# Kernel tuning notes

Hardware: AMD Instinct MI355X
Metric: run time of the kernel (lower is better)

## Reference

```python
import jax, jax.numpy as jnp
import numpy as np

# ---- constants mirroring init_kwargs ----
S = 128          # sheet_units
KA = 25          # aff_cf_units
C = 2            # aff_cf_channels
KL = 25          # lat_cf_units
EXC = 9          # exc_units
DA = 1           # aff_cf_dilation
DL = 1           # lat_cf_dilation
HOMEO_TARGET = 0.04
STRENGTH = 1.0

# ---- radial helper masks (get_circle / get_radial_cos) ----
def _dist(n):
    g = jnp.arange(n, dtype=jnp.float32) - (n - 1) / 2.0
    return jnp.sqrt(g[:, None] ** 2 + g[None, :] ** 2)

def _circle(n, r):
    return (_dist(n) < r).astype(jnp.float32)

def _rcos(n, wl):
    return jnp.cos(_dist(n) * jnp.pi / wl)

# afferent envelope: [C*KA*KA], channel-major like torch repeat+view
_ae = _rcos(KA, KA) ** 2 * _circle(KA, KA / 2)
_ae = _ae / _ae.max()
AFF_ENV = jnp.tile(_ae.reshape(1, KA * KA), (C, 1)).reshape(C * KA * KA)

# lateral (LRI) envelope: [KL*KL]
_inh = _rcos(KL, EXC / DL) ** 2 * _circle(KL, EXC / (2 * DL))
_le = _rcos(KL, KL) ** 2 * (1.0 - _inh) * _circle(KL, KL / 2)
LRI_ENV = (_le / _le.max()).reshape(KL * KL)

def _unfold(x, k, dil):
    """x: [C,H,W] -> patches [L, C*k*k], torch F.unfold ordering (C slowest)."""
    Cc, H, W = x.shape
    out = H - dil * (k - 1)
    idx = jnp.arange(out)[:, None] + dil * jnp.arange(k)[None, :]  # [out,k]
    p = x[:, idx, :]          # [C,out,k,W]
    p = p[:, :, :, idx]       # [C,out,k,out,k]
    p = p.transpose(1, 3, 0, 2, 4)  # [out_i,out_j,C,ki,kj]
    return p.reshape(out * out, Cc * k * k)

def setup_inputs() -> dict:
    key = jax.random.key(0)
    k1, k2 = jax.random.split(key)
    in_size = S + DA * (KA - 1)  # 152
    x = jax.random.uniform(k1, (1, C, in_size, in_size), dtype=jnp.float32)
    rfs = jax.random.uniform(k2, (S * S, C * KA * KA, 1), dtype=jnp.float32)
    rfs = rfs / rfs.sum(1, keepdims=True)
    lat_weights = jnp.ones((S * S, KL * KL, 1), jnp.float32) / (KL * KL)
    adathresh = jnp.zeros((1, 1, S, S), jnp.float32)
    return {"x": x, "rfs": rfs, "lat_weights": lat_weights, "adathresh": adathresh}

def _forward(x, rfs, lat_weights, adathresh):
    relu = jax.nn.relu
    rfs = relu(rfs)                 # no_grad positive clamp of params
    lw = relu(lat_weights)
    # afferent: unfold + envelope + per-pixel dot (bmm with [L,F,1])
    tiles = _unfold(x[0], KA, DA) * AFF_ENV[None, :]          # [L, C*KA*KA]
    raw_aff = jnp.einsum('lf,lf->l', tiles, rfs[:, :, 0]).reshape(S, S)
    aff = jax.lax.stop_gradient(raw_aff) - adathresh[0, 0]
    lat = relu(aff)
    # lateral inhibition: pad so unfold yields S*S positions
    p = DL * (KL - 1) // 2
    lt = _unfold(jnp.pad(lat, p)[None], KL, DL) * LRI_ENV[None, :]  # [L, KL*KL]
    lat_neg = jnp.einsum('lf,lf->l', lt, jax.lax.stop_gradient(lw)[:, :, 0]).reshape(S, S)
    lat = lat - lat_neg
    lat = jnp.tanh(relu(lat * STRENGTH + aff))
    # hebbian lateral correlations term (learning_flag path)
    lt2 = _unfold(jnp.pad(lat, p, constant_values=HOMEO_TARGET)[None], KL, DL) * LRI_ENV[None, :]
    weighted = lt2 * lat.reshape(S * S, 1)
    lat_correlations = jnp.einsum('lf,lf->', weighted, lw[:, :, 0])
    return (raw_aff.reshape(1, 1, S, S), lat.reshape(1, 1, S, S),
            lat_correlations, tiles[:, None, :])

def reference(x, rfs, lat_weights, adathresh):
    return _forward(x, rfs, lat_weights, adathresh)
```

## Files before the change

kernel.cpp:

```cpp
#include <hip/hip_runtime.h>
#include <math.h>

#define S 128
#define KA 25
#define KL 25
#define PATCH (KA * KA)
#define FEAT (2 * PATCH)
#define PI_F 3.14159265358979323846f

#define WS_ENV 0
#define WS_LAT0 640
#define WS_PART 17024

__global__ __launch_bounds__(256) void k_tiles_aff(const float* __restrict__ x,
                                                   const float* __restrict__ rfs,
                                                   const float* __restrict__ ada,
                                                   float* __restrict__ raw_aff,
                                                   float* __restrict__ tiles,
                                                   float* __restrict__ ws) {
    __shared__ float s_ae[PATCH];
    __shared__ float s_part[4];
    const int tid = threadIdx.x;
    const int lane = tid & 63;
    const int wv = tid >> 6;

    for (int i = tid; i < PATCH; i += 256) {
        float di = (float)(i / KA) - 12.0f;
        float dj = (float)(i % KA) - 12.0f;
        float d = sqrtf(di * di + dj * dj);
        float v = 0.0f;
        if (d < 12.5f) {
            float c = cosf(d * (PI_F / 25.0f));
            v = c * c;
        }
        s_ae[i] = v;
    }
    __syncthreads();

    const int l = blockIdx.x;
    const int li = l >> 7;
    const int lj = l & 127;
    const long base = (long)l * FEAT;

    float acc = 0.0f;
    for (int f = tid; f < FEAT; f += 256) {
        int c = (f >= PATCH) ? 1 : 0;
        int r = f - c * PATCH;
        int ki = r / KA;
        int kj = r - ki * KA;
        float xv = x[c * (152 * 152) + (li + ki) * 152 + (lj + kj)];
        float t = xv * s_ae[r];
        tiles[base + f] = t;
        acc += t * fmaxf(rfs[base + f], 0.0f);
    }

    for (int off = 32; off > 0; off >>= 1) acc += __shfl_down(acc, off);
    if (lane == 0) s_part[wv] = acc;
    __syncthreads();
    if (tid == 0) {
        float ra = s_part[0] + s_part[1] + s_part[2] + s_part[3];
        raw_aff[l] = ra;
        ws[WS_LAT0 + l] = fmaxf(ra - ada[l], 0.0f);
    }

    if (blockIdx.x == 0) {
        __syncthreads();
        float m = 0.0f;
        for (int i = tid; i < PATCH; i += 256) {
            float di = (float)(i / KL) - 12.0f;
            float dj = (float)(i % KL) - 12.0f;
            float d = sqrtf(di * di + dj * dj);
            float v = 0.0f;
            if (d < 12.5f) {
                float c1 = cosf(d * (PI_F / 25.0f));
                float inh = 0.0f;
                if (d < 4.5f) {
                    float c2 = cosf(d * (PI_F / 9.0f));
                    inh = c2 * c2;
                }
                v = c1 * c1 * (1.0f - inh);
            }
            s_ae[i] = v;
            m = fmaxf(m, v);
        }
        for (int off = 32; off > 0; off >>= 1) m = fmaxf(m, __shfl_down(m, off));
        if (lane == 0) s_part[wv] = m;
        __syncthreads();
        float inv = 1.0f / fmaxf(fmaxf(s_part[0], s_part[1]),
                                 fmaxf(s_part[2], s_part[3]));
        for (int i = tid; i < PATCH; i += 256) ws[WS_ENV + i] = s_ae[i] * inv;
    }
}

__global__ __launch_bounds__(256) void k_lat(const float* __restrict__ raw_aff,
                                             const float* __restrict__ ada,
                                             const float* __restrict__ lw,
                                             float* __restrict__ latf,
                                             const float* __restrict__ ws) {
    __shared__ float s_le[PATCH];
    const int tid = threadIdx.x;
    for (int i = tid; i < PATCH; i += 256) s_le[i] = ws[WS_ENV + i];
    __syncthreads();

    const int lane = tid & 63;
    const int wv = tid >> 6;
    const int l = blockIdx.x * 4 + wv;
    const int li = l >> 7;
    const int lj = l & 127;
    const long base = (long)l * PATCH;
    const float* __restrict__ lat0 = ws + WS_LAT0;

    float acc = 0.0f;
    for (int f = lane; f < PATCH; f += 64) {
        int ki = f / KL;
        int kj = f - ki * KL;
        int ri = li + ki - 12;
        int rj = lj + kj - 12;
        float lv = 0.0f;
        if (ri >= 0 && ri < S && rj >= 0 && rj < S) lv = lat0[ri * S + rj];
        acc += lv * s_le[f] * fmaxf(lw[base + f], 0.0f);
    }
    for (int off = 32; off > 0; off >>= 1) acc += __shfl_down(acc, off);

    if (lane == 0) {
        float aff_l = raw_aff[l] - ada[l];
        float lat0_l = fmaxf(aff_l, 0.0f);
        float v = (lat0_l - acc)  + aff_l;
        latf[l] = tanhf(fmaxf(v, 0.0f));
    }
}

__global__ __launch_bounds__(256) void k_corr(const float* __restrict__ latf,
                                              const float* __restrict__ lw,
                                              float* __restrict__ ws) {
    __shared__ float s_le[PATCH];
    __shared__ float s_part[4];
    const int tid = threadIdx.x;
    for (int i = tid; i < PATCH; i += 256) s_le[i] = ws[WS_ENV + i];
    __syncthreads();

    const int lane = tid & 63;
    const int wv = tid >> 6;
    const int l = blockIdx.x * 4 + wv;
    const int li = l >> 7;
    const int lj = l & 127;
    const long base = (long)l * PATCH;

    float acc = 0.0f;
    for (int f = lane; f < PATCH; f += 64) {
        int ki = f / KL;
        int kj = f - ki * KL;
        int ri = li + ki - 12;
        int rj = lj + kj - 12;
        float lv = 0.04f;
        if (ri >= 0 && ri < S && rj >= 0 && rj < S) lv = latf[ri * S + rj];
        acc += lv * s_le[f] * fmaxf(lw[base + f], 0.0f);
    }
    for (int off = 32; off > 0; off >>= 1) acc += __shfl_down(acc, off);

    if (lane == 0) s_part[wv] = acc * latf[l];
    __syncthreads();
    if (tid == 0)
        ws[WS_PART + blockIdx.x] = s_part[0] + s_part[1] + s_part[2] + s_part[3];
}

__global__ __launch_bounds__(256) void k_reduce(const float* __restrict__ ws,
                                                float* __restrict__ corr) {
    __shared__ float s_part[4];
    const int tid = threadIdx.x;
    const int lane = tid & 63;
    const int wv = tid >> 6;
    float acc = 0.0f;
    for (int i = tid; i < 4096; i += 256) acc += ws[WS_PART + i];
    for (int off = 32; off > 0; off >>= 1) acc += __shfl_down(acc, off);
    if (lane == 0) s_part[wv] = acc;
    __syncthreads();
    if (tid == 0) corr[0] = s_part[0] + s_part[1] + s_part[2] + s_part[3];
}

extern "C" void kernel_launch(void* const* d_in, const int* in_sizes, int n_in,
                              void* d_out, int out_size, void* d_ws, size_t ws_size,
                              hipStream_t stream) {
    const float* x   = (const float*)d_in[0];
    const float* rfs = (const float*)d_in[1];
    const float* lw  = (const float*)d_in[2];
    const float* ada = (const float*)d_in[3];

    float* out      = (float*)d_out;
    float* raw_aff  = out;
    float* latf     = out + S * S;
    float* corr     = out + 2 * S * S;
    float* tiles    = out + 2 * S * S + 1;
    float* ws       = (float*)d_ws;

    k_tiles_aff<<<S * S, 256, 0, stream>>>(x, rfs, ada, raw_aff, tiles, ws);
    k_lat<<<(S * S) / 4, 256, 0, stream>>>(raw_aff, ada, lw, latf, ws);
    k_corr<<<(S * S) / 4, 256, 0, stream>>>(latf, lw, ws);
    k_reduce<<<1, 256, 0, stream>>>(ws, corr);
}
```

Measured before the change: 229.7 us.

## Fuse all stages into one cooperative persistent kernel with vectorized loads

Replaces four kernel launches with a single cooperative kernel that uses grid-wide syncs between the afferent, lateral and correlation stages. Pixels are processed in pairs per wave so rfs and lateral weights can be read as float4, and zero- or target-padded lateral maps in workspace remove bounds checks. The tiles output is written separately with aligned float4 stores. The aim is lower launch overhead and better memory bandwidth use, at the cost of grid syncs, the reads of x done twice, and a dependence on all 1024 blocks being co-resident.

```diff
diff --git a/kernel.cpp b/kernel.cpp
--- a/kernel.cpp
+++ b/kernel.cpp
@@ -1,181 +1,271 @@
 #include <hip/hip_runtime.h>
+#include <hip/hip_cooperative_groups.h>
 #include <math.h>
+
+namespace cg = cooperative_groups;
 
 #define S 128
 #define KA 25
-#define KL 25
-#define PATCH (KA * KA)
-#define FEAT (2 * PATCH)
+#define PATCH 625
+#define FEAT 1250
 #define PI_F 3.14159265358979323846f
-
-#define WS_ENV 0
-#define WS_LAT0 640
-#define WS_PART 17024
-
-__global__ __launch_bounds__(256) void k_tiles_aff(const float* __restrict__ x,
-                                                   const float* __restrict__ rfs,
-                                                   const float* __restrict__ ada,
-                                                   float* __restrict__ raw_aff,
-                                                   float* __restrict__ tiles,
-                                                   float* __restrict__ ws) {
-    __shared__ float s_ae[PATCH];
-    __shared__ float s_part[4];
+#define PADW 152
+#define PADA (PADW * PADW)
+
+#define NBLK 1024
+#define NTHR 256
+#define NWAVE 4096
+#define NPAIR 8192
+
+#define WS_LAT0P 0
+#define WS_LATFP 23168
+#define WS_PART 46336
+
+#define NTILE 20480000
+#define NF4T 5119999
+
+__device__ __forceinline__ int div25(int r) { return (r * 10486) >> 18; }
+__device__ __forceinline__ int woff(int r) { return r + 127 * div25(r); }
+__device__ __forceinline__ int eslot(int r) { return (r & 3) * 160 + (r >> 2); }
+
+__global__ __launch_bounds__(NTHR, 4) void k_all(const float* __restrict__ x,
+                                                 const float* __restrict__ rfs,
+                                                 const float* __restrict__ lw,
+                                                 const float* __restrict__ ada,
+                                                 float* __restrict__ raw_aff,
+                                                 float* __restrict__ latf,
+                                                 float* __restrict__ corr,
+                                                 float* __restrict__ tiles,
+                                                 float* __restrict__ ws) {
+    cg::grid_group grid = cg::this_grid();
+    __shared__ float s_ae[640];
+    __shared__ float s_le[640];
+    __shared__ float s_red[4];
+
     const int tid = threadIdx.x;
     const int lane = tid & 63;
     const int wv = tid >> 6;
-
-    for (int i = tid; i < PATCH; i += 256) {
-        float di = (float)(i / KA) - 12.0f;
-        float dj = (float)(i % KA) - 12.0f;
+    const int bid = blockIdx.x;
+    const int gid = bid * NTHR + tid;
+    const int wid = bid * 4 + wv;
+
+    float m = 0.0f;
+    for (int r = tid; r < PATCH; r += NTHR) {
+        int qi = div25(r);
+        float di = (float)qi - 12.0f;
+        float dj = (float)(r - 25 * qi) - 12.0f;
         float d = sqrtf(di * di + dj * dj);
-        float v = 0.0f;
+        float ae = 0.0f, le = 0.0f;
         if (d < 12.5f) {
-            float c = cosf(d * (PI_F / 25.0f));
-            v = c * c;
-        }
-        s_ae[i] = v;
-    }
+            float c1 = cosf(d * (PI_F / 25.0f));
+            ae = c1 * c1;
+            float inh = 0.0f;
+            if (d < 4.5f) {
+                float c2 = cosf(d * (PI_F / 9.0f));
+                inh = c2 * c2;
+            }
+            le = c1 * c1 * (1.0f - inh);
+        }
+        s_ae[eslot(r)] = ae;
+        s_le[eslot(r)] = le;
+        m = fmaxf(m, le);
+    }
+    if (tid < 12) {
+        int q = tid / 3, t = 157 + tid - 3 * q;
+        s_ae[q * 160 + t] = 0.0f;
+        s_le[q * 160 + t] = 0.0f;
+    }
+    for (int o = 32; o; o >>= 1) m = fmaxf(m, __shfl_down(m, o));
+    if (!lane) s_red[wv] = m;
     __syncthreads();
-
-    const int l = blockIdx.x;
-    const int li = l >> 7;
-    const int lj = l & 127;
-    const long base = (long)l * FEAT;
-
-    float acc = 0.0f;
-    for (int f = tid; f < FEAT; f += 256) {
+    {
+        float inv = 1.0f / fmaxf(fmaxf(s_red[0], s_red[1]),
+                                 fmaxf(s_red[2], s_red[3]));
+        for (int s = tid; s < 640; s += NTHR) s_le[s] *= inv;
+    }
+    for (int i = gid; i < PADA; i += NBLK * NTHR) {
+        int pi = i / PADW, pj = i - pi * PADW;
+        if (pi < 12 || pi >= 140 || pj < 12 || pj >= 140) {
+            ws[WS_LAT0P + i] = 0.0f;
+            ws[WS_LATFP + i] = 0.04f;
+        }
+    }
+    __syncthreads();
+
+    for (int p = wid; p < NPAIR; p += NWAVE) {
+        const int l0 = 2 * p;
+        const int li = l0 >> 7, lj = l0 & 127;
+        const int wb = li * PADW + lj;
+        const long B = (long)l0 * FEAT;
+        float aA = 0.0f, aB = 0.0f;
+        for (int k = lane; k < 625; k += 64) {
+            const float4 rv = *reinterpret_cast<const float4*>(rfs + B + 4 * (long)k);
+#pragma unroll
+            for (int j = 0; j < 4; ++j) {
+                int f = 4 * k + j;
+                int row1 = (f >= FEAT) ? 1 : 0;
+                int g = f - row1 * FEAT;
+                int c = (g >= PATCH) ? 1 : 0;
+                int r = g - c * PATCH;
+                float t = x[c * PADA + wb + row1 + woff(r)] * s_ae[eslot(r)];
+                float v = t * fmaxf((&rv.x)[j], 0.0f);
+                aA += row1 ? 0.0f : v;
+                aB += row1 ? v : 0.0f;
+            }
+        }
+        for (int o = 32; o; o >>= 1) {
+            aA += __shfl_down(aA, o);
+            aB += __shfl_down(aB, o);
+        }
+        if (!lane) {
+            raw_aff[l0]     = aA;
+            raw_aff[l0 + 1] = aB;
+            int pc = (li + 12) * PADW + (lj + 12);
+            ws[WS_LAT0P + pc]     = fmaxf(aA - ada[l0],     0.0f);
+            ws[WS_LAT0P + pc + 1] = fmaxf(aB - ada[l0 + 1], 0.0f);
+        }
+    }
+
+    for (long k = gid; k < NF4T; k += (long)NBLK * NTHR) {
+        long i0 = 3 + (k << 2);
+        float4 v;
+#pragma unroll
+        for (int j = 0; j < 4; ++j) {
+            unsigned int e = (unsigned int)(i0 + j);
+            unsigned int l = e / 1250u;
+            int f = (int)(e - l * 1250u);
+            int c = (f >= PATCH) ? 1 : 0;
+            int r = f - c * PATCH;
+            int li2 = (int)(l >> 7), lj2 = (int)(l & 127u);
+            (&v.x)[j] = x[c * PADA + li2 * PADW + lj2 + woff(r)] * s_ae[eslot(r)];
+        }
+        *reinterpret_cast<float4*>(tiles + i0) = v;
+    }
+    if (gid < 4) {
+        unsigned int e = (gid < 3) ? (unsigned int)gid : (NTILE - 1u);
+        unsigned int l = e / 1250u;
+        int f = (int)(e - l * 1250u);
         int c = (f >= PATCH) ? 1 : 0;
         int r = f - c * PATCH;
-        int ki = r / KA;
-        int kj = r - ki * KA;
-        float xv = x[c * (152 * 152) + (li + ki) * 152 + (lj + kj)];
-        float t = xv * s_ae[r];
-        tiles[base + f] = t;
-        acc += t * fmaxf(rfs[base + f], 0.0f);
-    }
-
-    for (int off = 32; off > 0; off >>= 1) acc += __shfl_down(acc, off);
-    if (lane == 0) s_part[wv] = acc;
+        int li2 = (int)(l >> 7), lj2 = (int)(l & 127u);
+        tiles[e] = x[c * PADA + li2 * PADW + lj2 + woff(r)] * s_ae[eslot(r)];
+    }
+
+    grid.sync();
+
+    auto lat_pair = [&](int p) -> float2 {
+        const int l0 = 2 * p;
+        const int li = l0 >> 7, lj = l0 & 127;
+        const int wb = li * PADW + lj;
+        const long B = (long)p * FEAT;
+        const int peel = (p & 1) ? 2 : 0;
+        const float* __restrict__ plat0 = ws + WS_LAT0P;
+        float aA = 0.0f, aB = 0.0f;
+        if (lane < peel) {
+            int f = lane;
+            aA += plat0[wb + f] * s_le[eslot(f)] * fmaxf(lw[B + f], 0.0f);
+        }
+        for (int k = lane; k < 312; k += 64) {
+            int f0 = peel + 4 * k;
+            const float4 w4 = *reinterpret_cast<const float4*>(lw + B + f0);
+#pragma unroll
+            for (int j = 0; j < 4; ++j) {
+                int f = f0 + j;
+                int row1 = (f >= PATCH) ? 1 : 0;
+                int r = f - row1 * PATCH;
+                float gv = plat0[wb + row1 + woff(r)];
+                float v = gv * s_le[eslot(r)] * fmaxf((&w4.x)[j], 0.0f);
+                aA += row1 ? 0.0f : v;
+                aB += row1 ? v : 0.0f;
+            }
+        }
+        if (peel == 0 && lane < 2) {
+            int f = 1248 + lane;
+            int r = f - PATCH;
+            aB += plat0[wb + 1 + woff(r)] * s_le[eslot(r)] * fmaxf(lw[B + f], 0.0f);
+        }
+        for (int o = 32; o; o >>= 1) {
+            aA += __shfl_down(aA, o);
+            aB += __shfl_down(aB, o);
+        }
+        float2 lv = {0.0f, 0.0f};
+        if (!lane) {
+            float af0 = raw_aff[l0] - ada[l0];
+            float L0 = tanhf(fmaxf(fmaxf(af0, 0.0f) - aA + af0, 0.0f));
+            float af1 = raw_aff[l0 + 1] - ada[l0 + 1];
+            float L1 = tanhf(fmaxf(fmaxf(af1, 0.0f) - aB + af1, 0.0f));
+            latf[l0]     = L0;
+            latf[l0 + 1] = L1;
+            int pc = (li + 12) * PADW + (lj + 12);
+            ws[WS_LATFP + pc]     = L0;
+            ws[WS_LATFP + pc + 1] = L1;
+            lv.x = L0; lv.y = L1;
+        }
+        return lv;
+    };
+    const float2 lvA = lat_pair(wid);
+    const float2 lvB = lat_pair(wid + NWAVE);
+
+    grid.sync();
+
+    auto corr_pair = [&](int p) -> float2 {
+        const int l0 = 2 * p;
+        const int li = l0 >> 7, lj = l0 & 127;
+        const int wb = li * PADW + lj;
+        const long B = (long)p * FEAT;
+        const int peel = (p & 1) ? 2 : 0;
+        const float* __restrict__ platf = ws + WS_LATFP;
+        float aA = 0.0f, aB = 0.0f;
+        if (lane < peel) {
+            int f = lane;
+            aA += platf[wb + f] * s_le[eslot(f)] * fmaxf(lw[B + f], 0.0f);
+        }
+        for (int k = lane; k < 312; k += 64) {
+            int f0 = peel + 4 * k;
+            const float4 w4 = *reinterpret_cast<const float4*>(lw + B + f0);
+#pragma unroll
+            for (int j = 0; j < 4; ++j) {
+                int f = f0 + j;
+                int row1 = (f >= PATCH) ? 1 : 0;
+                int r = f - row1 * PATCH;
+                float gv = platf[wb + row1 + woff(r)];
+                float v = gv * s_le[eslot(r)] * fmaxf((&w4.x)[j], 0.0f);
+                aA += row1 ? 0.0f : v;
+                aB += row1 ? v : 0.0f;
+            }
+        }
+        if (peel == 0 && lane < 2) {
+            int f = 1248 + lane;
+            int r = f - PATCH;
+            aB += platf[wb + 1 + woff(r)] * s_le[eslot(r)] * fmaxf(lw[B + f], 0.0f);
+        }
+        for (int o = 32; o; o >>= 1) {
+            aA += __shfl_down(aA, o);
+            aB += __shfl_down(aB, o);
+        }
+        return {aA, aB};
+    };
+    const float2 cA = corr_pair(wid);
+    const float2 cB = corr_pair(wid + NWAVE);
+
+    float wsum = 0.0f;
+    if (!lane)
+        wsum = cA.x * lvA.x + cA.y * lvA.y + cB.x * lvB.x + cB.y * lvB.y;
+    if (!lane) s_red[wv] = wsum;
     __syncthreads();
-    if (tid == 0) {
-        float ra = s_part[0] + s_part[1] + s_part[2] + s_part[3];
-        raw_aff[l] = ra;
-        ws[WS_LAT0 + l] = fmaxf(ra - ada[l], 0.0f);
-    }
-
-    if (blockIdx.x == 0) {
+    if (!tid)
+        ws[WS_PART + bid] = s_red[0] + s_red[1] + s_red[2] + s_red[3];
+
+    grid.sync();
+
+    if (bid == 0) {
+        float a = 0.0f;
+        for (int i = tid; i < NBLK; i += NTHR) a += ws[WS_PART + i];
+        for (int o = 32; o; o >>= 1) a += __shfl_down(a, o);
+        if (!lane) s_red[wv] = a;
         __syncthreads();
-        float m = 0.0f;
-        for (int i = tid; i < PATCH; i += 256) {
-            float di = (float)(i / KL) - 12.0f;
-            float dj = (float)(i % KL) - 12.0f;
-            float d = sqrtf(di * di + dj * dj);
-            float v = 0.0f;
-            if (d < 12.5f) {
-                float c1 = cosf(d * (PI_F / 25.0f));
-                float inh = 0.0f;
-                if (d < 4.5f) {
-                    float c2 = cosf(d * (PI_F / 9.0f));
-                    inh = c2 * c2;
-                }
-                v = c1 * c1 * (1.0f - inh);
-            }
-            s_ae[i] = v;
-            m = fmaxf(m, v);
-        }
-        for (int off = 32; off > 0; off >>= 1) m = fmaxf(m, __shfl_down(m, off));
-        if (lane == 0) s_part[wv] = m;
-        __syncthreads();
-        float inv = 1.0f / fmaxf(fmaxf(s_part[0], s_part[1]),
-                                 fmaxf(s_part[2], s_part[3]));
-        for (int i = tid; i < PATCH; i += 256) ws[WS_ENV + i] = s_ae[i] * inv;
-    }
-}
-
-__global__ __launch_bounds__(256) void k_lat(const float* __restrict__ raw_aff,
-                                             const float* __restrict__ ada,
-                                             const float* __restrict__ lw,
-                                             float* __restrict__ latf,
-                                             const float* __restrict__ ws) {
-    __shared__ float s_le[PATCH];
-    const int tid = threadIdx.x;
-    for (int i = tid; i < PATCH; i += 256) s_le[i] = ws[WS_ENV + i];
-    __syncthreads();
-
-    const int lane = tid & 63;
-    const int wv = tid >> 6;
-    const int l = blockIdx.x * 4 + wv;
-    const int li = l >> 7;
-    const int lj = l & 127;
-    const long base = (long)l * PATCH;
-    const float* __restrict__ lat0 = ws + WS_LAT0;
-
-    float acc = 0.0f;
-    for (int f = lane; f < PATCH; f += 64) {
-        int ki = f / KL;
-        int kj = f - ki * KL;
-        int ri = li + ki - 12;
-        int rj = lj + kj - 12;
-        float lv = 0.0f;
-        if (ri >= 0 && ri < S && rj >= 0 && rj < S) lv = lat0[ri * S + rj];
-        acc += lv * s_le[f] * fmaxf(lw[base + f], 0.0f);
-    }
-    for (int off = 32; off > 0; off >>= 1) acc += __shfl_down(acc, off);
-
-    if (lane == 0) {
-        float aff_l = raw_aff[l] - ada[l];
-        float lat0_l = fmaxf(aff_l, 0.0f);
-        float v = (lat0_l - acc)  + aff_l;
-        latf[l] = tanhf(fmaxf(v, 0.0f));
-    }
-}
-
-__global__ __launch_bounds__(256) void k_corr(const float* __restrict__ latf,
-                                              const float* __restrict__ lw,
-                                              float* __restrict__ ws) {
-    __shared__ float s_le[PATCH];
-    __shared__ float s_part[4];
-    const int tid = threadIdx.x;
-    for (int i = tid; i < PATCH; i += 256) s_le[i] = ws[WS_ENV + i];
-    __syncthreads();
-
-    const int lane = tid & 63;
-    const int wv = tid >> 6;
-    const int l = blockIdx.x * 4 + wv;
-    const int li = l >> 7;
-    const int lj = l & 127;
-    const long base = (long)l * PATCH;
-
-    float acc = 0.0f;
-    for (int f = lane; f < PATCH; f += 64) {
-        int ki = f / KL;
-        int kj = f - ki * KL;
-        int ri = li + ki - 12;
-        int rj = lj + kj - 12;
-        float lv = 0.04f;
-        if (ri >= 0 && ri < S && rj >= 0 && rj < S) lv = latf[ri * S + rj];
-        acc += lv * s_le[f] * fmaxf(lw[base + f], 0.0f);
-    }
-    for (int off = 32; off > 0; off >>= 1) acc += __shfl_down(acc, off);
-
-    if (lane == 0) s_part[wv] = acc * latf[l];
-    __syncthreads();
-    if (tid == 0)
-        ws[WS_PART + blockIdx.x] = s_part[0] + s_part[1] + s_part[2] + s_part[3];
-}
-
-__global__ __launch_bounds__(256) void k_reduce(const float* __restrict__ ws,
-                                                float* __restrict__ corr) {
-    __shared__ float s_part[4];
-    const int tid = threadIdx.x;
-    const int lane = tid & 63;
-    const int wv = tid >> 6;
-    float acc = 0.0f;
-    for (int i = tid; i < 4096; i += 256) acc += ws[WS_PART + i];
-    for (int off = 32; off > 0; off >>= 1) acc += __shfl_down(acc, off);
-    if (lane == 0) s_part[wv] = acc;
-    __syncthreads();
-    if (tid == 0) corr[0] = s_part[0] + s_part[1] + s_part[2] + s_part[3];
+        if (!tid) corr[0] = s_red[0] + s_red[1] + s_red[2] + s_red[3];
+    }
 }
 
 extern "C" void kernel_launch(void* const* d_in, const int* in_sizes, int n_in,
@@ -193,8 +283,9 @@
     float* tiles    = out + 2 * S * S + 1;
     float* ws       = (float*)d_ws;
 
-    k_tiles_aff<<<S * S, 256, 0, stream>>>(x, rfs, ada, raw_aff, tiles, ws);
-    k_lat<<<(S * S) / 4, 256, 0, stream>>>(raw_aff, ada, lw, latf, ws);
-    k_corr<<<(S * S) / 4, 256, 0, stream>>>(latf, lw, ws);
-    k_reduce<<<1, 256, 0, stream>>>(ws, corr);
+    void* args[] = {(void*)&x, (void*)&rfs, (void*)&lw, (void*)&ada,
+                    (void*)&raw_aff, (void*)&latf, (void*)&corr,
+                    (void*)&tiles, (void*)&ws};
+    hipLaunchCooperativeKernel((const void*)k_all, dim3(NBLK), dim3(NTHR),
+                               args, 0, stream);
 }
```

Result: slower. 633.6 us (+175.9%).
